# Kernel tuning notes

Measured on AMD Instinct MI355X. Metric: run time of the kernel, lower is better.

Reference implementation:

```python
import jax, jax.numpy as jnp
import numpy as np

KH, KW = 3, 3

def setup_inputs() -> dict:
    key = jax.random.key(0)
    kx, kw = jax.random.split(key)
    X = jax.random.normal(kx, (4096, 8192), dtype=jnp.float32)
    # nn.Parameter(torch.rand(kernel_size)) -> uniform [0,1)
    weight = jax.random.uniform(kw, (KH, KW), dtype=jnp.float32)
    bias = jnp.zeros((1,), dtype=jnp.float32)
    return {"X": X, "weight": weight, "bias": bias}

def reference(X, weight, bias):
    # valid 2D cross-correlation (lax conv does correlation, no kernel flip)
    # X: [H, W]; weight: [kh, kw] -> out: [H-kh+1, W-kw+1]
    out = jax.lax.conv_general_dilated(
        X[None, None, :, :],            # NCHW, N=C=1
        weight[None, None, :, :],        # OIHW, O=I=1
        window_strides=(1, 1),
        padding="VALID",
    )[0, 0]
    return out + bias
```

## Files before the change

kernel.cpp:

```cpp
#include <hip/hip_runtime.h>

#define H   4096
#define W   8192
#define HO  4094
#define WO  8190
#define TWI 256
#define TWO 252
#define TH  16
#define IH  18
#define TPB 8
#define BLK 256

typedef __attribute__((address_space(3))) void       lds_void;
typedef __attribute__((address_space(1))) const void glob_void;

__global__ __launch_bounds__(BLK) void ConvLayer_4140348473931_kernel(
    const float* __restrict__ X, const float* __restrict__ Wt,
    const float* __restrict__ Bias, float* __restrict__ Out)
{
    __shared__ float bufA[IH][TWI];
    __shared__ float bufB[IH][TWI];

    const int tid  = threadIdx.x;
    const int lane = tid & 63;
    const int wav  = tid >> 6;

    const int Cbase = blockIdx.x * TWO;
    const int Rblk  = blockIdx.y * (TPB * TH);

    const int gcol = min(Cbase + 4 * lane, W - 4);

    float w[9];
#pragma unroll
    for (int i = 0; i < 9; ++i) w[i] = Wt[i];
    const float bias = Bias[0];

    const int lr = wav * 4;
    const int lc = lane * 4;
    const int oc = Cbase + lc;

#define STAGE(BUF, R0)                                                        \
    do {                                                                      \
        _Pragma("unroll")                                                     \
        for (int k = 0; k < 5; ++k) {                                         \
            const int rr = wav + 4 * k;                                       \
            if (rr < IH) {                                                    \
                int gr = (R0) + rr; if (gr > H - 1) gr = H - 1;               \
                const float* src = X + (size_t)gr * W + gcol;                 \
                __builtin_amdgcn_global_load_lds(                             \
                    (glob_void*)src, (lds_void*)&(BUF)[rr][0], 16, 0, 0);     \
            }                                                                 \
        }                                                                     \
    } while (0)

#define WAITN()                                                               \
    do { if (wav < 2) asm volatile("s_waitcnt vmcnt(5)" ::: "memory");        \
         else         asm volatile("s_waitcnt vmcnt(4)" ::: "memory"); } while (0)
#define WAIT0() asm volatile("s_waitcnt vmcnt(0)" ::: "memory")
#define FENCE() asm volatile("" ::: "memory")
#define BAR()   do { __builtin_amdgcn_s_barrier(); FENCE(); } while (0)

#define CSTORE(BUF, R0)                                                       \
    do {                                                                      \
        float acc[4][4];                                                      \
        _Pragma("unroll") for (int i = 0; i < 4; ++i)                         \
        _Pragma("unroll") for (int j = 0; j < 4; ++j) acc[i][j] = bias;       \
        _Pragma("unroll")                                                     \
        for (int ir = 0; ir < 6; ++ir) {                                      \
            float4 a4 = *reinterpret_cast<const float4*>(&(BUF)[lr + ir][lc]);\
            float2 b2 = *reinterpret_cast<const float2*>(&(BUF)[lr + ir][lc + 4]); \
            const float xw[6] = {a4.x, a4.y, a4.z, a4.w, b2.x, b2.y};         \
            _Pragma("unroll")                                                 \
            for (int i = 0; i < 4; ++i) {                                     \
                const int kh = ir - i;                                        \
                if (kh >= 0 && kh < 3) {                                      \
                    _Pragma("unroll")                                         \
                    for (int j = 0; j < 4; ++j) {                             \
                        float s = acc[i][j];                                  \
                        s = fmaf(w[kh * 3 + 0], xw[j + 0], s);                \
                        s = fmaf(w[kh * 3 + 1], xw[j + 1], s);                \
                        s = fmaf(w[kh * 3 + 2], xw[j + 2], s);                \
                        acc[i][j] = s;                                        \
                    }                                                         \
                }                                                             \
            }                                                                 \
        }                                                                     \
        if (lane < 63) {                                                      \
            _Pragma("unroll")                                                 \
            for (int i = 0; i < 4; ++i) {                                     \
                const int r = (R0) + lr + i;                                  \
                if (r < HO) {                                                 \
                    float* orow = Out + (size_t)r * WO + oc;                  \
                    if (oc + 2 <= WO)                                         \
                        *reinterpret_cast<float2*>(orow) = make_float2(acc[i][0], acc[i][1]); \
                    if (oc + 4 <= WO)                                         \
                        *reinterpret_cast<float2*>(orow + 2) = make_float2(acc[i][2], acc[i][3]); \
                }                                                             \
            }                                                                 \
        }                                                                     \
    } while (0)

    STAGE(bufA, Rblk);
#pragma unroll
    for (int t = 0; t < TPB; t += 2) {
        const int R0 = Rblk + t * TH;

        if (t + 1 < TPB) { STAGE(bufB, R0 + TH); WAITN(); } else { WAIT0(); }
        BAR();
        CSTORE(bufA, R0);
        FENCE(); BAR();

        if (t + 2 < TPB) { STAGE(bufA, R0 + 2 * TH); WAITN(); } else { WAIT0(); }
        BAR();
        CSTORE(bufB, R0 + TH);
        FENCE(); BAR();
    }

#undef STAGE
#undef WAITN
#undef WAIT0
#undef FENCE
#undef BAR
#undef CSTORE
}

extern "C" void kernel_launch(void* const* d_in, const int* in_sizes, int n_in,
                              void* d_out, int out_size, void* d_ws, size_t ws_size,
                              hipStream_t stream) {
    const float* X    = (const float*)d_in[0];
    const float* Wt   = (const float*)d_in[1];
    const float* Bias = (const float*)d_in[2];
    float* Out        = (float*)d_out;

    dim3 block(BLK);
    dim3 grid((WO + TWO - 1) / TWO,
              (HO + TPB * TH - 1) / (TPB * TH));
    ConvLayer_4140348473931_kernel<<<grid, block, 0, stream>>>(X, Wt, Bias, Out);
}
```

Baseline: 53.07 us.

## Convert conv kernel to persistent grid-stride tile loop with double buffering

```diff
diff --git a/kernel.cpp b/kernel.cpp
--- a/kernel.cpp
+++ b/kernel.cpp
@@ -1,15 +1,18 @@
 #include <hip/hip_runtime.h>
 
-#define H   4096
-#define W   8192
-#define HO  4094
-#define WO  8190
-#define TWI 256
-#define TWO 252
-#define TH  16
-#define IH  18
-#define TPB 8
-#define BLK 256
+#define H    4096
+#define W    8192
+#define HO   4094
+#define WO   8190
+#define TWI  256
+#define TWO  252
+#define TH   16
+#define IH   18
+#define NCT  33
+#define NBT  256
+#define NT   (NCT * NBT)
+#define NBLK 512
+#define BLK  256
 
 typedef __attribute__((address_space(3))) void       lds_void;
 typedef __attribute__((address_space(1))) const void glob_void;
@@ -25,11 +28,6 @@
     const int lane = tid & 63;
     const int wav  = tid >> 6;
 
-    const int Cbase = blockIdx.x * TWO;
-    const int Rblk  = blockIdx.y * (TPB * TH);
-
-    const int gcol = min(Cbase + 4 * lane, W - 4);
-
     float w[9];
 #pragma unroll
     for (int i = 0; i < 9; ++i) w[i] = Wt[i];
@@ -37,38 +35,38 @@
 
     const int lr = wav * 4;
     const int lc = lane * 4;
-    const int oc = Cbase + lc;
 
-#define STAGE(BUF, R0)                                                        \
+#define STAGE(BUFP, T)                                                        \
     do {                                                                      \
+        const int _band = (T) / NCT;                                          \
+        const int _ct   = (T) - _band * NCT;                                  \
+        const int _R0   = _band * TH;                                         \
+        const int _gc   = min(_ct * TWO + 4 * lane, W - 4);                   \
         _Pragma("unroll")                                                     \
         for (int k = 0; k < 5; ++k) {                                         \
             const int rr = wav + 4 * k;                                       \
             if (rr < IH) {                                                    \
-                int gr = (R0) + rr; if (gr > H - 1) gr = H - 1;               \
-                const float* src = X + (size_t)gr * W + gcol;                 \
+                int gr = _R0 + rr; if (gr > H - 1) gr = H - 1;                \
+                const float* src = X + (size_t)gr * W + _gc;                  \
                 __builtin_amdgcn_global_load_lds(                             \
-                    (glob_void*)src, (lds_void*)&(BUF)[rr][0], 16, 0, 0);     \
+                    (glob_void*)src, (lds_void*)&(BUFP)[rr][0], 16, 0, 0);    \
             }                                                                 \
         }                                                                     \
     } while (0)
 
-#define WAITN()                                                               \
-    do { if (wav < 2) asm volatile("s_waitcnt vmcnt(5)" ::: "memory");        \
-         else         asm volatile("s_waitcnt vmcnt(4)" ::: "memory"); } while (0)
-#define WAIT0() asm volatile("s_waitcnt vmcnt(0)" ::: "memory")
-#define FENCE() asm volatile("" ::: "memory")
-#define BAR()   do { __builtin_amdgcn_s_barrier(); FENCE(); } while (0)
-
-#define CSTORE(BUF, R0)                                                       \
+#define CSTORE(BUFP, T)                                                       \
     do {                                                                      \
+        const int _band = (T) / NCT;                                          \
+        const int _ct   = (T) - _band * NCT;                                  \
+        const int _R0   = _band * TH;                                         \
+        const int _oc   = _ct * TWO + lc;                                     \
         float acc[4][4];                                                      \
         _Pragma("unroll") for (int i = 0; i < 4; ++i)                         \
         _Pragma("unroll") for (int j = 0; j < 4; ++j) acc[i][j] = bias;       \
         _Pragma("unroll")                                                     \
         for (int ir = 0; ir < 6; ++ir) {                                      \
-            float4 a4 = *reinterpret_cast<const float4*>(&(BUF)[lr + ir][lc]);\
-            float2 b2 = *reinterpret_cast<const float2*>(&(BUF)[lr + ir][lc + 4]); \
+            float4 a4 = *reinterpret_cast<const float4*>(&(BUFP)[lr + ir][lc]); \
+            float2 b2 = *reinterpret_cast<const float2*>(&(BUFP)[lr + ir][lc + 4]); \
             const float xw[6] = {a4.x, a4.y, a4.z, a4.w, b2.x, b2.y};         \
             _Pragma("unroll")                                                 \
             for (int i = 0; i < 4; ++i) {                                     \
@@ -88,39 +86,45 @@
         if (lane < 63) {                                                      \
             _Pragma("unroll")                                                 \
             for (int i = 0; i < 4; ++i) {                                     \
-                const int r = (R0) + lr + i;                                  \
+                const int r = _R0 + lr + i;                                   \
                 if (r < HO) {                                                 \
-                    float* orow = Out + (size_t)r * WO + oc;                  \
-                    if (oc + 2 <= WO)                                         \
+                    float* orow = Out + (size_t)r * WO + _oc;                 \
+                    if (_oc + 2 <= WO)                                        \
                         *reinterpret_cast<float2*>(orow) = make_float2(acc[i][0], acc[i][1]); \
-                    if (oc + 4 <= WO)                                         \
+                    if (_oc + 4 <= WO)                                        \
                         *reinterpret_cast<float2*>(orow + 2) = make_float2(acc[i][2], acc[i][3]); \
                 }                                                             \
             }                                                                 \
         }                                                                     \
     } while (0)
 
-    STAGE(bufA, Rblk);
-#pragma unroll
-    for (int t = 0; t < TPB; t += 2) {
-        const int R0 = Rblk + t * TH;
+    int T = (int)blockIdx.x;
+    STAGE(bufA, T);
+    int cur = 0;
+    while (true) {
+        const int Tn = T + NBLK;
+        float (*bc)[TWI] = cur ? bufB : bufA;
+        float (*bn)[TWI] = cur ? bufA : bufB;
 
-        if (t + 1 < TPB) { STAGE(bufB, R0 + TH); WAITN(); } else { WAIT0(); }
-        BAR();
-        CSTORE(bufA, R0);
-        FENCE(); BAR();
+        if (Tn < NT) {
+            STAGE(bn, Tn);
+            if (wav < 2) asm volatile("s_waitcnt vmcnt(5)" ::: "memory");
+            else         asm volatile("s_waitcnt vmcnt(4)" ::: "memory");
+        } else {
+            asm volatile("s_waitcnt vmcnt(0)" ::: "memory");
+        }
+        __builtin_amdgcn_s_barrier();
 
-        if (t + 2 < TPB) { STAGE(bufA, R0 + 2 * TH); WAITN(); } else { WAIT0(); }
-        BAR();
-        CSTORE(bufB, R0 + TH);
-        FENCE(); BAR();
+        CSTORE(bc, T);
+
+        asm volatile("" ::: "memory");
+        __builtin_amdgcn_s_barrier();
+
+        if (Tn >= NT) break;
+        T = Tn; cur ^= 1;
     }
 
 #undef STAGE
-#undef WAITN
-#undef WAIT0
-#undef FENCE
-#undef BAR
 #undef CSTORE
 }
 
@@ -133,7 +137,6 @@
     float* Out        = (float*)d_out;
 
     dim3 block(BLK);
-    dim3 grid((WO + TWO - 1) / TWO,
-              (HO + TPB * TH - 1) / (TPB * TH));
+    dim3 grid(NBLK);
     ConvLayer_4140348473931_kernel<<<grid, block, 0, stream>>>(X, Wt, Bias, Out);
 }
```

Result: faster. 51.18 us (-3.6%).
